# Kernel optimization log

Hardware: AMD Instinct MI355X
Metric: run time of the kernel (lower is better)

## Reference

```python
import jax, jax.numpy as jnp
import numpy as np

N_NODES = 50000
N_EDGES = 800000
IN_F, HID, OUT_F = 256, 128, 64
ATTN_SLOPE = 0.2   # DGL GATConv negative_slope default
ACT_SLOPE = 0.01   # nn.LeakyReLU default


def setup_inputs() -> dict:
    key = jax.random.key(0)
    ks = jax.random.split(key, 7)
    x = jax.random.normal(ks[0], (N_NODES, IN_F), dtype=jnp.float32)
    src = jax.random.randint(ks[1], (N_EDGES,), 0, N_NODES, dtype=jnp.int32)
    dst = jax.random.randint(ks[2], (N_EDGES,), 0, N_NODES, dtype=jnp.int32)
    W_gat = jax.random.normal(ks[3], (IN_F, HID), dtype=jnp.float32) * (1.0 / np.sqrt(IN_F))
    attn_l = jax.random.normal(ks[4], (HID,), dtype=jnp.float32) * 0.1
    attn_r = jax.random.normal(ks[5], (HID,), dtype=jnp.float32) * 0.1
    bias_gat = jnp.zeros((HID,), dtype=jnp.float32)
    W_lin = jax.random.normal(ks[6], (OUT_F, HID), dtype=jnp.float32) * (1.0 / np.sqrt(HID))
    return {"x": x, "src": src, "dst": dst, "W_gat": W_gat, "attn_l": attn_l,
            "attn_r": attn_r, "bias_gat": bias_gat, "W_lin": W_lin}


def reference(x, src, dst, W_gat, attn_l, attn_r, bias_gat, W_lin):
    N = x.shape[0]
    # GATConv (num_heads=1): linear projection then additive attention
    feat = x @ W_gat                         # [N, HID]
    el = feat @ attn_l                        # [N]  (sum(feat * a_l, -1))
    er = feat @ attn_r                        # [N]
    # per-edge logits, leaky_relu(0.2)
    e = jax.nn.leaky_relu(el[src] + er[dst], negative_slope=ATTN_SLOPE)  # [E]
    # segment softmax over edges grouped by destination node
    e_max = jax.ops.segment_max(e, dst, num_segments=N)  # [N] (-inf for isolated)
    alpha = jnp.exp(e - e_max[dst])                      # [E]
    denom = jax.ops.segment_sum(alpha, dst, num_segments=N)
    a = alpha / denom[dst]                               # [E]
    # scatter-weighted aggregation of source features
    msg = a[:, None] * feat[src]                         # [E, HID]
    agg = jax.ops.segment_sum(msg, dst, num_segments=N) + bias_gat  # [N, HID]
    # outer wrapper: LeakyReLU(0.01), squeeze (head dim already gone), linear no bias
    gene = jax.nn.leaky_relu(agg, negative_slope=ACT_SLOPE)
    return gene @ W_lin.T                                # [N, OUT_F]
```

## Files before the change

### kernel.cpp

```cpp
#include <hip/hip_runtime.h>
#include <hip/hip_bf16.h>


#define NNODES 50000
#define NEDGES 800000
#define IN_F   256
#define HID    128
#define OUTF   64

#define PA_EPT   8
#define PA_EDGES (256 * PA_EPT)
#define PA_NB    ((NEDGES + PA_EDGES - 1) / PA_EDGES)
#define NBKT     ((NNODES + 255) / 256)
#define BCAP     5120
#define NSTRIP   (NNODES / 16)
#define GB       ((NSTRIP + 3) / 4)

#define AGN      64
#define AGSLOT   64
#define AGB      784

typedef unsigned short u16;
typedef unsigned long long u64;
typedef __bf16 bf16x8 __attribute__((ext_vector_type(8)));
typedef float  f32x4  __attribute__((ext_vector_type(4)));

__device__ __forceinline__ u16 f2b(float f) {
    union { float f; unsigned u; } v; v.f = f;
    unsigned u = v.u;
    return (u16)((u + 0x7fffu + ((u >> 16) & 1u)) >> 16);
}
__device__ __forceinline__ float b2f_lo(unsigned v) {
    union { unsigned u; float f; } c; c.u = (v & 0xffffu) << 16; return c.f;
}
__device__ __forceinline__ float b2f_hi(unsigned v) {
    union { unsigned u; float f; } c; c.u = v & 0xffff0000u; return c.f;
}
__device__ __forceinline__ float lrelu02_exp(float t) {
    t = t > 0.f ? t : 0.2f * t;
    return __expf(t);
}

__global__ __launch_bounds__(256) void pack0(const float* __restrict__ Wg,
                                             const float* __restrict__ Wl,
                                             u16* __restrict__ pWg,
                                             u16* __restrict__ pWl,
                                             int* __restrict__ bcnt) {
    int blk = blockIdx.x, tid = threadIdx.x;
    if (blk < 16) {
        int t = blk * 256 + tid;
        int lane = t & 63, tile = t >> 6;
        int nt = tile & 7, kt = tile >> 3;
        int col = lane & 15, quad = lane >> 4;
        int krow = kt * 32 + quad * 8;
        int ncol = nt * 16 + col;
#pragma unroll
        for (int j = 0; j < 8; j++) pWg[t * 8 + j] = f2b(Wg[(krow + j) * HID + ncol]);
    } else if (blk < 20) {
        int t = (blk - 16) * 256 + tid;
        int lane = t & 63, tile = t >> 6;
        int nt = tile & 3, kt = tile >> 2;
        int col = lane & 15, quad = lane >> 4;
        int o  = nt * 16 + col;
        int k0 = kt * 32 + quad * 8;
#pragma unroll
        for (int j = 0; j < 8; j++) pWl[t * 8 + j] = f2b(Wl[o * HID + k0 + j]);
    } else {
        if (tid < NBKT) bcnt[tid] = 0;
    }
}

__global__ __launch_bounds__(256) void k_mega(
        const float* __restrict__ x, const u16* __restrict__ pWg,
        const float* __restrict__ al_, const float* __restrict__ ar_,
        unsigned* __restrict__ feat2, float* __restrict__ el, float* __restrict__ er,
        const int* __restrict__ src, const int* __restrict__ dst,
        int* __restrict__ bcnt, u64* __restrict__ pairs) {
    __shared__ u64 smemU[21504 / 8];
    char* smem = (char*)smemU;
    int blk = blockIdx.x, tid = threadIdx.x;

    if (blk < GB) {
        int wave = tid >> 6, lane = tid & 63;
        int strip = blk * 4 + wave;
        bool valid = (strip < NSTRIP);
        int m0 = strip * 16;
        int col = lane & 15, quad = lane >> 4;

        f32x4 xa[16];
        if (valid) {
            const float* xr = x + (size_t)(m0 + col) * IN_F + quad * 8;
#pragma unroll
            for (int kt = 0; kt < 8; kt++) {
                xa[2 * kt]     = *reinterpret_cast<const f32x4*>(xr + kt * 32);
                xa[2 * kt + 1] = *reinterpret_cast<const f32x4*>(xr + kt * 32 + 4);
            }
            asm volatile("" :: "v"(xa[0]), "v"(xa[1]), "v"(xa[2]), "v"(xa[3]),
                               "v"(xa[4]), "v"(xa[5]), "v"(xa[6]), "v"(xa[7]),
                               "v"(xa[8]), "v"(xa[9]), "v"(xa[10]), "v"(xa[11]),
                               "v"(xa[12]), "v"(xa[13]), "v"(xa[14]), "v"(xa[15]));
        }
        bf16x8 av[8];
        if (valid) {
#pragma unroll
            for (int kt = 0; kt < 8; kt++)
#pragma unroll
                for (int j = 0; j < 4; j++) {
                    av[kt][j]     = (__bf16)xa[2 * kt][j];
                    av[kt][4 + j] = (__bf16)xa[2 * kt + 1][j];
                }
        }

        f32x4 acc[8] = {};
        for (int c = 0; c < 4; c++) {
#pragma unroll
            for (int i = 0; i < 4; i++) {
                f32x4 w = *reinterpret_cast<const f32x4*>(
                    (const char*)pWg + c * 16384 + i * 4096 + tid * 16);
                *reinterpret_cast<f32x4*>(smem + i * 4096 + tid * 16) = w;
            }
            __syncthreads();
            if (valid) {
#pragma unroll
                for (int kt2 = 0; kt2 < 2; kt2++) {
                    int kt = c * 2 + kt2;
#pragma unroll
                    for (int nt = 0; nt < 8; nt++) {
                        bf16x8 b = *reinterpret_cast<const bf16x8*>(
                            smem + ((kt2 * 8 + nt) * 64 + lane) * 16);
                        acc[nt] = __builtin_amdgcn_mfma_f32_16x16x32_bf16(av[kt], b, acc[nt], 0, 0, 0);
                    }
                }
            }
            __syncthreads();
        }

        if (!valid) return;
        float pl[4] = {0, 0, 0, 0}, pr[4] = {0, 0, 0, 0};
#pragma unroll
        for (int nt = 0; nt < 8; nt++) {
            float alv = al_[nt * 16 + col], arv = ar_[nt * 16 + col];
#pragma unroll
            for (int reg = 0; reg < 4; reg++) {
                pl[reg] += acc[nt][reg] * alv;
                pr[reg] += acc[nt][reg] * arv;
            }
        }
#pragma unroll
        for (int m = 1; m < 16; m <<= 1)
#pragma unroll
            for (int reg = 0; reg < 4; reg++) {
                pl[reg] += __shfl_xor(pl[reg], m, 64);
                pr[reg] += __shfl_xor(pr[reg], m, 64);
            }
        if (col == 0) {
#pragma unroll
            for (int reg = 0; reg < 4; reg++) {
                el[m0 + quad * 4 + reg] = pl[reg];
                er[m0 + quad * 4 + reg] = pr[reg];
            }
        }
#pragma unroll
        for (int nt = 0; nt < 8; nt++)
#pragma unroll
            for (int reg = 0; reg < 4; reg++) {
                u16* fp = (u16*)feat2;
                fp[(size_t)(m0 + quad * 4 + reg) * HID + nt * 16 + col] = f2b(acc[nt][reg]);
            }
        return;
    }

    int* hist    = (int*)smem;
    int* binbase = hist + 256;
    int* gbase   = binbase + 256;
    int* fill    = gbase + 256;
    int* stmp    = fill + 256;
    u64* spair   = (u64*)(smem + 5120);

    int e0 = (blk - GB) * PA_EDGES;
    int cnt = NEDGES - e0; if (cnt > PA_EDGES) cnt = PA_EDGES;

    hist[tid] = 0; fill[tid] = 0;
    __syncthreads();

    int es[PA_EPT], ed[PA_EPT];
#pragma unroll
    for (int j = 0; j < PA_EPT; j++) {
        int idx = e0 + j * 256 + tid;
        if (idx < NEDGES) {
            es[j] = src[idx];
            ed[j] = dst[idx];
            atomicAdd(&hist[ed[j] >> 8], 1);
        } else ed[j] = -1;
    }
    __syncthreads();

    stmp[tid] = (tid < NBKT) ? hist[tid] : 0;
    __syncthreads();
#pragma unroll
    for (int ofs = 1; ofs < 256; ofs <<= 1) {
        int u = (tid >= ofs) ? stmp[tid - ofs] : 0;
        __syncthreads();
        stmp[tid] += u;
        __syncthreads();
    }
    if (tid < NBKT) {
        binbase[tid] = stmp[tid] - hist[tid];
        if (hist[tid] > 0)
            gbase[tid] = tid * BCAP + atomicAdd(&bcnt[tid], hist[tid]);
    }
    __syncthreads();

#pragma unroll
    for (int j = 0; j < PA_EPT; j++) {
        if (ed[j] >= 0) {
            int b = ed[j] >> 8;
            int r = atomicAdd(&fill[b], 1);
            int loc = binbase[b] + r;
            spair[loc] = ((u64)(unsigned)ed[j] << 32) | (unsigned)es[j];
        }
    }
    __syncthreads();

    for (int i = tid; i < cnt; i += 256) {
        u64 p = spair[i];
        int b = (int)(p >> 40);
        pairs[gbase[b] + (i - binbase[b])] = p;
    }
}

__global__ __launch_bounds__(1024) void k_agg64(const u64* __restrict__ pairs,
                                                const int* __restrict__ bcnt,
                                                const float* __restrict__ el,
                                                const float* __restrict__ er,
                                                const unsigned* __restrict__ feat2,
                                                const float* __restrict__ bias,
                                                const u16* __restrict__ pWl,
                                                float* __restrict__ out) {
    __shared__ int   cnt_l[AGN];
    __shared__ float erl[AGN];
    __shared__ int   ssrc[AGN * AGSLOT];
    __shared__ float swgt[AGN * AGSLOT];
    __shared__ unsigned sg[AGN * 68];

    int tid = threadIdx.x;
    int wave = tid >> 6, lane = tid & 63;
    int logical = (blockIdx.x & 7) * 98 + (blockIdx.x >> 3);
    int nb = logical * AGN;
    if (nb >= NNODES) return;
    int cb = logical >> 2;

    if (tid < AGN) {
        cnt_l[tid] = 0;
        int n = nb + tid;
        erl[tid] = (n < NNODES) ? er[n] : 0.f;
    }
    __syncthreads();

    int cntb = bcnt[cb];
    const u64* reg = pairs + (size_t)cb * BCAP;
    for (int i = tid; i < cntb; i += 1024) {
        u64 p = reg[i];
        int d = (int)(unsigned)(p >> 32);
        unsigned dl = (unsigned)(d - nb);
        if (dl < (unsigned)AGN) {
            int s = (int)(unsigned)(p & 0xffffffffu);
            float w = lrelu02_exp(el[s] + erl[dl]);
            int slot = atomicAdd(&cnt_l[dl], 1);
            if (slot < AGSLOT) {
                ssrc[dl * AGSLOT + slot] = s;
                swgt[dl * AGSLOT + slot] = w;
            }
        }
    }
    __syncthreads();

    float bl = bias[lane * 2 + 0], bh = bias[lane * 2 + 1];
    for (int i = 0; i < 4; i++) {
        int dl = wave * 4 + i;
        int cnt = cnt_l[dl]; if (cnt > AGSLOT) cnt = AGSLOT;
        const int*   ep = ssrc + dl * AGSLOT;
        const float* wp = swgt + dl * AGSLOT;

        float p0 = 0.f, p1 = 0.f, q0 = 0.f, q1 = 0.f;
        float r0 = 0.f, r1 = 0.f, t0 = 0.f, t1 = 0.f;
        float u0 = 0.f, u1 = 0.f, x0 = 0.f, x1 = 0.f;
        float y0 = 0.f, y1 = 0.f, z0 = 0.f, z1 = 0.f;
        float dn = 0.f;
        int j = 0;
        for (; j + 8 <= cnt; j += 8) {
            int4 sa = *reinterpret_cast<const int4*>(ep + j);
            int4 sb = *reinterpret_cast<const int4*>(ep + j + 4);
            float4 wa = *reinterpret_cast<const float4*>(wp + j);
            float4 wb = *reinterpret_cast<const float4*>(wp + j + 4);
            unsigned v0 = feat2[(size_t)sa.x * 64 + lane];
            unsigned v1 = feat2[(size_t)sa.y * 64 + lane];
            unsigned v2 = feat2[(size_t)sa.z * 64 + lane];
            unsigned v3 = feat2[(size_t)sa.w * 64 + lane];
            unsigned v4 = feat2[(size_t)sb.x * 64 + lane];
            unsigned v5 = feat2[(size_t)sb.y * 64 + lane];
            unsigned v6 = feat2[(size_t)sb.z * 64 + lane];
            unsigned v7 = feat2[(size_t)sb.w * 64 + lane];
            asm volatile("" :: "v"(v0), "v"(v1), "v"(v2), "v"(v3),
                               "v"(v4), "v"(v5), "v"(v6), "v"(v7));
            p0 += wa.x * b2f_lo(v0); p1 += wa.x * b2f_hi(v0);
            q0 += wa.y * b2f_lo(v1); q1 += wa.y * b2f_hi(v1);
            r0 += wa.z * b2f_lo(v2); r1 += wa.z * b2f_hi(v2);
            t0 += wa.w * b2f_lo(v3); t1 += wa.w * b2f_hi(v3);
            u0 += wb.x * b2f_lo(v4); u1 += wb.x * b2f_hi(v4);
            x0 += wb.y * b2f_lo(v5); x1 += wb.y * b2f_hi(v5);
            y0 += wb.z * b2f_lo(v6); y1 += wb.z * b2f_hi(v6);
            z0 += wb.w * b2f_lo(v7); z1 += wb.w * b2f_hi(v7);
            dn += ((wa.x + wa.y) + (wa.z + wa.w)) + ((wb.x + wb.y) + (wb.z + wb.w));
        }
        if (j + 4 <= cnt) {
            int4 sa = *reinterpret_cast<const int4*>(ep + j);
            float4 wa = *reinterpret_cast<const float4*>(wp + j);
            unsigned v0 = feat2[(size_t)sa.x * 64 + lane];
            unsigned v1 = feat2[(size_t)sa.y * 64 + lane];
            unsigned v2 = feat2[(size_t)sa.z * 64 + lane];
            unsigned v3 = feat2[(size_t)sa.w * 64 + lane];
            asm volatile("" :: "v"(v0), "v"(v1), "v"(v2), "v"(v3));
            p0 += wa.x * b2f_lo(v0); p1 += wa.x * b2f_hi(v0);
            q0 += wa.y * b2f_lo(v1); q1 += wa.y * b2f_hi(v1);
            r0 += wa.z * b2f_lo(v2); r1 += wa.z * b2f_hi(v2);
            t0 += wa.w * b2f_lo(v3); t1 += wa.w * b2f_hi(v3);
            dn += (wa.x + wa.y) + (wa.z + wa.w);
            j += 4;
        }
        for (; j < cnt; j++) {
            int s = ep[j];
            float w = wp[j];
            unsigned v = feat2[(size_t)s * 64 + lane];
            p0 += w * b2f_lo(v); p1 += w * b2f_hi(v);
            dn += w;
        }
        float a0 = ((p0 + q0) + (r0 + t0)) + ((u0 + x0) + (y0 + z0));
        float a1 = ((p1 + q1) + (r1 + t1)) + ((u1 + x1) + (y1 + z1));

        float inv = dn > 0.f ? 1.f / dn : 0.f;
        float g0 = a0 * inv + bl;
        float g1 = a1 * inv + bh;
        g0 = g0 > 0.f ? g0 : 0.01f * g0;
        g1 = g1 > 0.f ? g1 : 0.01f * g1;
        sg[dl * 68 + lane] = (unsigned)f2b(g0) | ((unsigned)f2b(g1) << 16);
    }
    __syncthreads();

    int col = lane & 15, quad = lane >> 4;
    int tile = wave >> 2;
    int nt = wave & 3;
    f32x4 acc = {};
#pragma unroll
    for (int kt = 0; kt < 4; kt++) {
        bf16x8 a = *reinterpret_cast<const bf16x8*>(&sg[(tile * 16 + col) * 68 + kt * 16 + quad * 4]);
        bf16x8 bf = *reinterpret_cast<const bf16x8*>(pWl + ((kt * 4 + nt) * 64 + lane) * 8);
        acc = __builtin_amdgcn_mfma_f32_16x16x32_bf16(a, bf, acc, 0, 0, 0);
    }
#pragma unroll
    for (int reg = 0; reg < 4; reg++) {
        int row = nb + tile * 16 + quad * 4 + reg;
        if (row < NNODES)
            out[(size_t)row * OUTF + nt * 16 + col] = acc[reg];
    }
}

extern "C" void kernel_launch(void* const* d_in, const int* in_sizes, int n_in,
                              void* d_out, int out_size, void* d_ws, size_t ws_size,
                              hipStream_t stream) {
    const float* x      = (const float*)d_in[0];
    const int*   src    = (const int*)d_in[1];
    const int*   dst    = (const int*)d_in[2];
    const float* Wg     = (const float*)d_in[3];
    const float* attn_l = (const float*)d_in[4];
    const float* attn_r = (const float*)d_in[5];
    const float* bias   = (const float*)d_in[6];
    const float* Wl     = (const float*)d_in[7];
    float* out          = (float*)d_out;

    char* ws = (char*)d_ws;
    size_t off = 0;
    auto alloc = [&](size_t b) { size_t r = off; off += (b + 255) & ~(size_t)255; return r; };
    size_t pwgOff  = alloc((size_t)8 * 8 * 64 * 8 * 2);
    size_t pwlOff  = alloc((size_t)4 * 4 * 64 * 8 * 2);
    size_t featOff = alloc((size_t)NNODES * HID * 2);
    size_t elOff   = alloc((size_t)NNODES * 4);
    size_t erOff   = alloc((size_t)NNODES * 4);
    size_t pairOff = alloc((size_t)NBKT * BCAP * 8);
    size_t bcntOff = alloc((size_t)NBKT * 4);

    u16*      pWg   = (u16*)(ws + pwgOff);
    u16*      pWl   = (u16*)(ws + pwlOff);
    unsigned* feat2 = (unsigned*)(ws + featOff);
    float*    el    = (float*)(ws + elOff);
    float*    er    = (float*)(ws + erOff);
    u64*      pairs = (u64*)(ws + pairOff);
    int*      bcnt  = (int*)(ws + bcntOff);

    pack0<<<21, 256, 0, stream>>>(Wg, Wl, pWg, pWl, bcnt);
    k_mega<<<GB + PA_NB, 256, 0, stream>>>(x, pWg, attn_l, attn_r, feat2, el, er,
                                           src, dst, bcnt, pairs);
    k_agg64<<<AGB, 1024, 0, stream>>>(pairs, bcnt, el, er, feat2, bias,
                                      pWl, out);
}
```

Measured before the change: 154.5 us.

## Use 64-node edge buckets and scatter pairs directly without LDS staging

Edge buckets shrink from 256 to 64 destination nodes, so each aggregation block reads exactly its own bucket instead of scanning a bucket four times larger and filtering. The partition kernel drops its prefix scan and shared-memory staging of pairs and writes each pair straight to global memory at its reserved offset. This trades the coalesced bucket-ordered writes for scattered 8-byte global stores, and it issues more global atomics on bcnt (782 buckets). The per-bucket capacity of 1536 is tighter against overflow.

```diff
diff --git a/kernel.cpp b/kernel.cpp
--- a/kernel.cpp
+++ b/kernel.cpp
@@ -11,8 +11,8 @@
 #define PA_EPT   8
 #define PA_EDGES (256 * PA_EPT)
 #define PA_NB    ((NEDGES + PA_EDGES - 1) / PA_EDGES)
-#define NBKT     ((NNODES + 255) / 256)
-#define BCAP     5120
+#define NBKT     ((NNODES + 63) / 64)
+#define BCAP     1536
 #define NSTRIP   (NNODES / 16)
 #define GB       ((NSTRIP + 3) / 4)
 
@@ -66,7 +66,7 @@
 #pragma unroll
         for (int j = 0; j < 8; j++) pWl[t * 8 + j] = f2b(Wl[o * HID + k0 + j]);
     } else {
-        if (tid < NBKT) bcnt[tid] = 0;
+        for (int i = tid; i < NBKT; i += 256) bcnt[i] = 0;
     }
 }
 
@@ -76,7 +76,7 @@
         unsigned* __restrict__ feat2, float* __restrict__ el, float* __restrict__ er,
         const int* __restrict__ src, const int* __restrict__ dst,
         int* __restrict__ bcnt, u64* __restrict__ pairs) {
-    __shared__ u64 smemU[21504 / 8];
+    __shared__ u64 smemU[16384 / 8];
     char* smem = (char*)smemU;
     int blk = blockIdx.x, tid = threadIdx.x;
 
@@ -170,17 +170,13 @@
         return;
     }
 
-    int* hist    = (int*)smem;
-    int* binbase = hist + 256;
-    int* gbase   = binbase + 256;
-    int* fill    = gbase + 256;
-    int* stmp    = fill + 256;
-    u64* spair   = (u64*)(smem + 5120);
+    int* hist = (int*)smem;
+    int* gb   = hist + 1024;
+    int* fill = gb + 1024;
 
     int e0 = (blk - GB) * PA_EDGES;
-    int cnt = NEDGES - e0; if (cnt > PA_EDGES) cnt = PA_EDGES;
-
-    hist[tid] = 0; fill[tid] = 0;
+
+    for (int i = tid; i < 1024; i += 256) { hist[i] = 0; fill[i] = 0; }
     __syncthreads();
 
     int es[PA_EPT], ed[PA_EPT];
@@ -190,42 +186,26 @@
         if (idx < NEDGES) {
             es[j] = src[idx];
             ed[j] = dst[idx];
-            atomicAdd(&hist[ed[j] >> 8], 1);
+            atomicAdd(&hist[ed[j] >> 6], 1);
         } else ed[j] = -1;
     }
     __syncthreads();
 
-    stmp[tid] = (tid < NBKT) ? hist[tid] : 0;
-    __syncthreads();
-#pragma unroll
-    for (int ofs = 1; ofs < 256; ofs <<= 1) {
-        int u = (tid >= ofs) ? stmp[tid - ofs] : 0;
-        __syncthreads();
-        stmp[tid] += u;
-        __syncthreads();
-    }
-    if (tid < NBKT) {
-        binbase[tid] = stmp[tid] - hist[tid];
-        if (hist[tid] > 0)
-            gbase[tid] = tid * BCAP + atomicAdd(&bcnt[tid], hist[tid]);
+#pragma unroll
+    for (int k = 0; k < 4; k++) {
+        int b = tid * 4 + k;
+        int h = hist[b];
+        if (h > 0) gb[b] = b * BCAP + atomicAdd(&bcnt[b], h);
     }
     __syncthreads();
 
 #pragma unroll
     for (int j = 0; j < PA_EPT; j++) {
         if (ed[j] >= 0) {
-            int b = ed[j] >> 8;
+            int b = ed[j] >> 6;
             int r = atomicAdd(&fill[b], 1);
-            int loc = binbase[b] + r;
-            spair[loc] = ((u64)(unsigned)ed[j] << 32) | (unsigned)es[j];
-        }
-    }
-    __syncthreads();
-
-    for (int i = tid; i < cnt; i += 256) {
-        u64 p = spair[i];
-        int b = (int)(p >> 40);
-        pairs[gbase[b] + (i - binbase[b])] = p;
+            pairs[gb[b] + r] = ((u64)(unsigned)ed[j] << 32) | (unsigned)es[j];
+        }
     }
 }
 
@@ -248,7 +228,7 @@
     int logical = (blockIdx.x & 7) * 98 + (blockIdx.x >> 3);
     int nb = logical * AGN;
     if (nb >= NNODES) return;
-    int cb = logical >> 2;
+    int cb = logical;
 
     if (tid < AGN) {
         cnt_l[tid] = 0;
```

Result: slower. 173.8 us (+12.5%).
